# Kernel optimization log

Hardware: AMD Instinct MI355X
Metric: run time of the kernel (lower is better)

Reference implementation:

```python
import jax, jax.numpy as jnp
import numpy as np

CE_WEIGHT = 1.0
TRIPLET_WEIGHT = 0.1
MARGIN = 0.2


def setup_inputs() -> dict:
    key = jax.random.key(0)
    k1, k2, k3 = jax.random.split(key, 3)
    B, D, V = 4096, 512, 6000
    logits = jax.random.normal(k1, (B, V), dtype=jnp.float32)
    embeddings = jax.random.normal(k2, (B, D), dtype=jnp.float32)
    labels = jax.random.randint(k3, (B,), 0, 512, dtype=jnp.int64)
    return {"logits": logits, "embeddings": embeddings, "labels": labels}


def _pairwise_dist(emb):
    # Euclidean cdist via gram matrix; safe sqrt (zero grad where d2 == 0).
    sq = jnp.sum(emb * emb, axis=-1)  # [B]
    d2 = sq[:, None] + sq[None, :] - 2.0 * (emb @ emb.T)  # [B, B]
    d2 = jnp.maximum(d2, 0.0)
    safe = jnp.where(d2 > 0.0, d2, 1.0)
    return jnp.where(d2 > 0.0, jnp.sqrt(safe), 0.0)


def _losses(logits, embeddings, labels):
    B = logits.shape[0]
    # Cross entropy (mean reduction, matching nn.CrossEntropyLoss).
    logp = jax.nn.log_softmax(logits, axis=-1)
    ce_loss = -jnp.mean(jnp.take_along_axis(logp, labels[:, None], axis=1)[:, 0])

    # Batch-hard triplet loss, fully vectorized (one masked amax/amin per row).
    dist = _pairwise_dist(embeddings)  # [B, B]
    same = labels[:, None] == labels[None, :]  # [B, B]
    eye = jnp.eye(B, dtype=bool)
    pos_mask = same & ~eye
    neg_mask = ~same
    neg_inf = jnp.float32(-np.inf)
    pos_inf = jnp.float32(np.inf)
    hardest_pos = jnp.max(jnp.where(pos_mask, dist, neg_inf), axis=1)  # [B]
    hardest_neg = jnp.min(jnp.where(neg_mask, dist, pos_inf), axis=1)  # [B]
    valid = jnp.any(pos_mask, axis=1) & jnp.any(neg_mask, axis=1)  # [B]
    per_row = jax.nn.relu(hardest_pos - hardest_neg + MARGIN)
    per_row = jnp.where(valid, per_row, 0.0)
    n_valid = jnp.sum(valid.astype(jnp.float32))
    triplet_loss = jnp.where(n_valid > 0, jnp.sum(per_row) / jnp.maximum(n_valid, 1.0), 0.0)

    total_loss = CE_WEIGHT * ce_loss + TRIPLET_WEIGHT * triplet_loss
    return total_loss, ce_loss, triplet_loss


def reference(logits, embeddings, labels):
    return _losses(logits, embeddings, labels)
```

## Files before the change

kernel.cpp:

```cpp
#include <hip/hip_runtime.h>
#include <hip/hip_bf16.h>
#include <math.h>

#define BN   4096
#define DN   512
#define VN   6000
#define NCLS 512

typedef __attribute__((ext_vector_type(8)))  short short8;
typedef __attribute__((ext_vector_type(16))) float f32x16;

__device__ __forceinline__ unsigned short f2bf(float x) {
  unsigned int u = __float_as_uint(x);
  u = (u + 0x7FFFu + ((u >> 16) & 1u)) >> 16;
  return (unsigned short)u;
}

__device__ __forceinline__ void gld_lds16(const unsigned short* g, unsigned short* l) {
  __builtin_amdgcn_global_load_lds(
      (const __attribute__((address_space(1))) void*)g,
      (__attribute__((address_space(3))) void*)l, 16, 0, 0);
}

__launch_bounds__(256)
__global__ void prep_kernel(const float* __restrict__ emb, const int* __restrict__ labels,
                            unsigned short* __restrict__ embh, float* __restrict__ sqn,
                            int* __restrict__ cnt, int* __restrict__ posb,
                            int* __restrict__ negb) {
  const int row  = blockIdx.x * 4 + (threadIdx.x >> 6);
  const int lane = threadIdx.x & 63;
  const float4* rp = (const float4*)(emb + (size_t)row * DN);
  float4 a = rp[lane];
  float4 b = rp[lane + 64];
  float ss = a.x * a.x + a.y * a.y + a.z * a.z + a.w * a.w
           + b.x * b.x + b.y * b.y + b.z * b.z + b.w * b.w;
  ushort4 ha, hb;
  ha.x = f2bf(a.x); ha.y = f2bf(a.y); ha.z = f2bf(a.z); ha.w = f2bf(a.w);
  hb.x = f2bf(b.x); hb.y = f2bf(b.y); hb.z = f2bf(b.z); hb.w = f2bf(b.w);
  ushort4* wp = (ushort4*)(embh + (size_t)row * DN);
  wp[lane] = ha;
  wp[lane + 64] = hb;
#pragma unroll
  for (int off = 1; off < 64; off <<= 1) ss += __shfl_xor(ss, off);
  if (lane == 0) {
    sqn[row] = ss;
    posb[row] = 0;
    negb[row] = 0x7F800000;
    atomicAdd(cnt + labels[row], 1);
  }
}

__device__ __forceinline__ void triplet_job(int t, unsigned short* smem,
                                            const unsigned short* __restrict__ embh,
                                            const float* __restrict__ sqn,
                                            const int* __restrict__ labels,
                                            int* __restrict__ posb,
                                            int* __restrict__ negb, int lane) {
  const int m = lane & 31;
  const int half = lane >> 5;

  int J = (int)((sqrtf(8.f * (float)t + 1.f) - 1.f) * 0.5f);
  while ((J + 1) * (J + 2) / 2 <= t) ++J;
  while (J * (J + 1) / 2 > t) --J;
  const int I = t - J * (J + 1) / 2;
  const int i0 = I * 64, j0 = J * 64;
  const bool diag = (I == J);

  const int   li = labels[i0 + lane];
  const float qi = sqn[i0 + lane];
  const int   lj = labels[j0 + lane];
  const float qj = sqn[j0 + lane];

  const int lrow = lane >> 3;
  const int lchk = (lane & 7) ^ lrow;
  const unsigned short* gA = embh + (size_t)(i0 + lrow) * DN + lchk * 8;
  const unsigned short* gB = embh + (size_t)(j0 + lrow) * DN + lchk * 8;

  f32x16 acc[2][2] = {};
  f32x16 accT[2][2] = {};

#pragma unroll
  for (int s = 0; s < 8; ++s) {
    gld_lds16(gA + (size_t)s * 8 * DN, smem + s * 512);
    gld_lds16(gB + (size_t)s * 8 * DN, smem + 4096 + s * 512);
  }

  for (int ks = 0; ks < 8; ++ks) {
    const int cur = (ks & 1) * 8192;
    if (ks < 7) {
      const int nxt = 8192 - cur;
      const int kk = (ks + 1) * 64;
      asm volatile("s_waitcnt lgkmcnt(0)" ::: "memory");
#pragma unroll
      for (int s = 0; s < 8; ++s) {
        gld_lds16(gA + kk + (size_t)s * 8 * DN, smem + nxt + s * 512);
        gld_lds16(gB + kk + (size_t)s * 8 * DN, smem + nxt + 4096 + s * 512);
      }
      asm volatile("s_waitcnt vmcnt(16)" ::: "memory");
    } else {
      asm volatile("s_waitcnt vmcnt(0)" ::: "memory");
    }
    unsigned short* sA = smem + cur;
    unsigned short* sB = smem + cur + 4096;
#pragma unroll
    for (int q = 0; q < 4; ++q) {
      const int c = q * 2 + half;
      const int sw = ((c ^ (m & 7)) * 8);
      short8 a0 = *(const short8*)&sA[m * 64 + sw];
      short8 a1 = *(const short8*)&sA[(32 + m) * 64 + sw];
      short8 b0 = *(const short8*)&sB[m * 64 + sw];
      short8 b1 = *(const short8*)&sB[(32 + m) * 64 + sw];
      acc[0][0]  = __builtin_amdgcn_mfma_f32_32x32x16_bf16(a0, b0, acc[0][0], 0, 0, 0);
      acc[0][1]  = __builtin_amdgcn_mfma_f32_32x32x16_bf16(a0, b1, acc[0][1], 0, 0, 0);
      acc[1][0]  = __builtin_amdgcn_mfma_f32_32x32x16_bf16(a1, b0, acc[1][0], 0, 0, 0);
      acc[1][1]  = __builtin_amdgcn_mfma_f32_32x32x16_bf16(a1, b1, acc[1][1], 0, 0, 0);
      accT[0][0] = __builtin_amdgcn_mfma_f32_32x32x16_bf16(b0, a0, accT[0][0], 0, 0, 0);
      accT[0][1] = __builtin_amdgcn_mfma_f32_32x32x16_bf16(b0, a1, accT[0][1], 0, 0, 0);
      accT[1][0] = __builtin_amdgcn_mfma_f32_32x32x16_bf16(b1, a0, accT[1][0], 0, 0, 0);
      accT[1][1] = __builtin_amdgcn_mfma_f32_32x32x16_bf16(b1, a1, accT[1][1], 0, 0, 0);
    }
  }

  int*   sLab = (int*)smem;
  float* sQn  = (float*)(smem + 256);
  sLab[lane] = li;  sLab[64 + lane] = lj;
  sQn[lane]  = qi;  sQn[64 + lane]  = qj;
  asm volatile("s_waitcnt lgkmcnt(0)" ::: "memory");

  {
    const int gj0 = j0 + m, gj1 = j0 + 32 + m;
    const int cl0 = sLab[64 + m], cl1 = sLab[64 + 32 + m];
    const float cq0 = sQn[64 + m], cq1 = sQn[64 + 32 + m];
    float p0 = 0.f, p1 = 0.f, n0 = INFINITY, n1 = INFINITY;
#pragma unroll
    for (int rb = 0; rb < 2; ++rb) {
#pragma unroll
      for (int r = 0; r < 16; ++r) {
        const int ri = rb * 32 + (r & 3) + 8 * (r >> 2) + 4 * half;
        const int gi = i0 + ri;
        const int rl = sLab[ri];
        const float rq = sQn[ri];
        const float d0 = fmaf(-2.f, acc[rb][0][r], rq + cq0);
        const float d1 = fmaf(-2.f, acc[rb][1][r], rq + cq1);
        if (rl == cl0) { if (gi != gj0) p0 = fmaxf(p0, d0); } else n0 = fminf(n0, d0);
        if (rl == cl1) { if (gi != gj1) p1 = fmaxf(p1, d1); } else n1 = fminf(n1, d1);
      }
    }
    p0 = fmaxf(p0, __shfl_xor(p0, 32)); n0 = fminf(n0, __shfl_xor(n0, 32));
    p1 = fmaxf(p1, __shfl_xor(p1, 32)); n1 = fminf(n1, __shfl_xor(n1, 32));
    if (half == 0) {
      atomicMax(posb + gj0, __float_as_int(p0));
      atomicMin(negb + gj0, __float_as_int(n0));
      atomicMax(posb + gj1, __float_as_int(p1));
      atomicMin(negb + gj1, __float_as_int(n1));
    }
  }

  if (!diag) {
    const int gj0 = i0 + m, gj1 = i0 + 32 + m;
    const int cl0 = sLab[m], cl1 = sLab[32 + m];
    const float cq0 = sQn[m], cq1 = sQn[32 + m];
    float p0 = 0.f, p1 = 0.f, n0 = INFINITY, n1 = INFINITY;
#pragma unroll
    for (int rb = 0; rb < 2; ++rb) {
#pragma unroll
      for (int r = 0; r < 16; ++r) {
        const int rj = rb * 32 + (r & 3) + 8 * (r >> 2) + 4 * half;
        const int rl = sLab[64 + rj];
        const float rq = sQn[64 + rj];
        const float d0 = fmaf(-2.f, accT[rb][0][r], rq + cq0);
        const float d1 = fmaf(-2.f, accT[rb][1][r], rq + cq1);
        if (rl == cl0) p0 = fmaxf(p0, d0); else n0 = fminf(n0, d0);
        if (rl == cl1) p1 = fmaxf(p1, d1); else n1 = fminf(n1, d1);
      }
    }
    p0 = fmaxf(p0, __shfl_xor(p0, 32)); n0 = fminf(n0, __shfl_xor(n0, 32));
    p1 = fmaxf(p1, __shfl_xor(p1, 32)); n1 = fminf(n1, __shfl_xor(n1, 32));
    if (half == 0) {
      atomicMax(posb + gj0, __float_as_int(p0));
      atomicMin(negb + gj0, __float_as_int(n0));
      atomicMax(posb + gj1, __float_as_int(p1));
      atomicMin(negb + gj1, __float_as_int(n1));
    }
  }
}

__launch_bounds__(64, 2)
__global__ void fused_kernel(const float* __restrict__ logits,
                             const int* __restrict__ labels,
                             float* __restrict__ ce_part,
                             const unsigned short* __restrict__ embh,
                             const float* __restrict__ sqn,
                             int* __restrict__ posb, int* __restrict__ negb) {
  __shared__ unsigned short smem[16384];
  const int b = blockIdx.x;
  const int lane = threadIdx.x;

  int trip_job, ce_row;
  if (b < 32) {
    trip_job = 2048 + b; ce_row = -1;
  } else {
    const int g = (b - 32) / 3, r = (b - 32) % 3;
    if (r == 0) { trip_job = g; ce_row = -1; }
    else        { trip_job = -1; ce_row = g * 2 + (r - 1); }
  }

  if (trip_job >= 0) {
    triplet_job(trip_job, smem, embh, sqn, labels, posb, negb, lane);
    return;
  }

  const float* rp = logits + (size_t)ce_row * VN;
  const float xlab = rp[labels[ce_row]];
  const float4* q = (const float4*)rp;
  float4 v[24];
#pragma unroll
  for (int u = 0; u < 23; ++u) v[u] = q[lane + u * 64];
  if (lane < 28) v[23] = q[lane + 23 * 64];
  float s = 0.f;
#pragma unroll
  for (int u = 0; u < 23; ++u)
    s += __expf(v[u].x) + __expf(v[u].y) + __expf(v[u].z) + __expf(v[u].w);
  if (lane < 28)
    s += __expf(v[23].x) + __expf(v[23].y) + __expf(v[23].z) + __expf(v[23].w);
#pragma unroll
  for (int off = 1; off < 64; off <<= 1) s += __shfl_xor(s, off);
  if (lane == 0) ce_part[ce_row] = logf(s) - xlab;
}

__launch_bounds__(1024)
__global__ void finalize_kernel(const int* __restrict__ posb, const int* __restrict__ negb,
                                const int* __restrict__ labels, const int* __restrict__ cnt,
                                const float* __restrict__ ce_part, float* __restrict__ out) {
  const int tid = threadIdx.x;
  float cesum = 0.f, sum = 0.f, nv = 0.f;
#pragma unroll
  for (int u = 0; u < 4; ++u) {
    const int i = tid + u * 1024;
    cesum += ce_part[i];
    int c = cnt[labels[i]];
    float p = sqrtf(fmaxf(__int_as_float(posb[i]), 0.f));
    float n = sqrtf(fmaxf(__int_as_float(negb[i]), 0.f));
    float t = fmaxf(p - n + 0.2f, 0.f);
    if (c >= 2 && c < BN) { sum += t; nv += 1.f; }
  }
#pragma unroll
  for (int off = 1; off < 64; off <<= 1) {
    cesum += __shfl_xor(cesum, off);
    sum   += __shfl_xor(sum, off);
    nv    += __shfl_xor(nv, off);
  }
  __shared__ float s0[16], s1[16], s2[16];
  if ((tid & 63) == 0) { s0[tid >> 6] = cesum; s1[tid >> 6] = sum; s2[tid >> 6] = nv; }
  __syncthreads();
  if (tid == 0) {
    cesum = 0.f; sum = 0.f; nv = 0.f;
#pragma unroll
    for (int wv = 0; wv < 16; ++wv) { cesum += s0[wv]; sum += s1[wv]; nv += s2[wv]; }
    float trip = (nv > 0.f) ? sum / nv : 0.f;
    float ce = cesum * (1.f / BN);
    out[0] = ce + 0.1f * trip;
    out[1] = ce;
    out[2] = trip;
  }
}

extern "C" void kernel_launch(void* const* d_in, const int* in_sizes, int n_in,
                              void* d_out, int out_size, void* d_ws, size_t ws_size,
                              hipStream_t stream) {
  const float* logits = (const float*)d_in[0];
  const float* emb    = (const float*)d_in[1];
  const int*   labels = (const int*)d_in[2];
  float* out = (float*)d_out;

  char* ws = (char*)d_ws;
  unsigned short* embh = (unsigned short*)ws;
  float* sqn    = (float*)(ws + (size_t)BN * DN * 2);
  int*   posb   = (int*)((char*)sqn  + (size_t)BN * 4);
  int*   negb   = (int*)((char*)posb + (size_t)BN * 4);
  int*   cnt    = (int*)((char*)negb + (size_t)BN * 4);
  float* ce_part = (float*)((char*)cnt + (size_t)NCLS * 4);

  hipMemsetAsync(cnt, 0, (size_t)NCLS * 4, stream);
  hipLaunchKernelGGL(prep_kernel, dim3(BN / 4), dim3(256), 0, stream,
                     emb, labels, embh, sqn, cnt, posb, negb);
  hipLaunchKernelGGL(fused_kernel, dim3(32 + 2048 * 3), dim3(64), 0, stream,
                     logits, labels, ce_part, embh, sqn, posb, negb);
  hipLaunchKernelGGL(finalize_kernel, dim3(1), dim3(1024), 0, stream,
                     posb, negb, labels, cnt, ce_part, out);
}
```

Before: 179.2 us.

## Load MFMA operands directly from global into registers, drop LDS staging

The triplet Gram tile no longer stages bf16 embedding chunks through double-buffered LDS via global_load_lds. Each lane now loads its MFMA fragments straight from global memory into registers, with a 4-step software prefetch ring. LDS shrinks from 32KB to 1KB, which could allow more blocks to reside per CU. The cost is many short 16-byte strided global loads per lane instead of coalesced row loads, plus heavier register pressure from the fragment arrays.

```diff
diff --git a/kernel.cpp b/kernel.cpp
--- a/kernel.cpp
+++ b/kernel.cpp
@@ -14,12 +14,6 @@
   unsigned int u = __float_as_uint(x);
   u = (u + 0x7FFFu + ((u >> 16) & 1u)) >> 16;
   return (unsigned short)u;
-}
-
-__device__ __forceinline__ void gld_lds16(const unsigned short* g, unsigned short* l) {
-  __builtin_amdgcn_global_load_lds(
-      (const __attribute__((address_space(1))) void*)g,
-      (__attribute__((address_space(3))) void*)l, 16, 0, 0);
 }
 
 __launch_bounds__(256)
@@ -71,55 +65,40 @@
   const int   lj = labels[j0 + lane];
   const float qj = sqn[j0 + lane];
 
-  const int lrow = lane >> 3;
-  const int lchk = (lane & 7) ^ lrow;
-  const unsigned short* gA = embh + (size_t)(i0 + lrow) * DN + lchk * 8;
-  const unsigned short* gB = embh + (size_t)(j0 + lrow) * DN + lchk * 8;
+  const unsigned short* pa0 = embh + (size_t)(i0 + m)      * DN + half * 8;
+  const unsigned short* pa1 = embh + (size_t)(i0 + 32 + m) * DN + half * 8;
+  const unsigned short* pb0 = embh + (size_t)(j0 + m)      * DN + half * 8;
+  const unsigned short* pb1 = embh + (size_t)(j0 + 32 + m) * DN + half * 8;
 
   f32x16 acc[2][2] = {};
   f32x16 accT[2][2] = {};
 
-#pragma unroll
-  for (int s = 0; s < 8; ++s) {
-    gld_lds16(gA + (size_t)s * 8 * DN, smem + s * 512);
-    gld_lds16(gB + (size_t)s * 8 * DN, smem + 4096 + s * 512);
-  }
-
-  for (int ks = 0; ks < 8; ++ks) {
-    const int cur = (ks & 1) * 8192;
-    if (ks < 7) {
-      const int nxt = 8192 - cur;
-      const int kk = (ks + 1) * 64;
-      asm volatile("s_waitcnt lgkmcnt(0)" ::: "memory");
-#pragma unroll
-      for (int s = 0; s < 8; ++s) {
-        gld_lds16(gA + kk + (size_t)s * 8 * DN, smem + nxt + s * 512);
-        gld_lds16(gB + kk + (size_t)s * 8 * DN, smem + nxt + 4096 + s * 512);
-      }
-      asm volatile("s_waitcnt vmcnt(16)" ::: "memory");
-    } else {
-      asm volatile("s_waitcnt vmcnt(0)" ::: "memory");
-    }
-    unsigned short* sA = smem + cur;
-    unsigned short* sB = smem + cur + 4096;
-#pragma unroll
-    for (int q = 0; q < 4; ++q) {
-      const int c = q * 2 + half;
-      const int sw = ((c ^ (m & 7)) * 8);
-      short8 a0 = *(const short8*)&sA[m * 64 + sw];
-      short8 a1 = *(const short8*)&sA[(32 + m) * 64 + sw];
-      short8 b0 = *(const short8*)&sB[m * 64 + sw];
-      short8 b1 = *(const short8*)&sB[(32 + m) * 64 + sw];
-      acc[0][0]  = __builtin_amdgcn_mfma_f32_32x32x16_bf16(a0, b0, acc[0][0], 0, 0, 0);
-      acc[0][1]  = __builtin_amdgcn_mfma_f32_32x32x16_bf16(a0, b1, acc[0][1], 0, 0, 0);
-      acc[1][0]  = __builtin_amdgcn_mfma_f32_32x32x16_bf16(a1, b0, acc[1][0], 0, 0, 0);
-      acc[1][1]  = __builtin_amdgcn_mfma_f32_32x32x16_bf16(a1, b1, acc[1][1], 0, 0, 0);
-      accT[0][0] = __builtin_amdgcn_mfma_f32_32x32x16_bf16(b0, a0, accT[0][0], 0, 0, 0);
-      accT[0][1] = __builtin_amdgcn_mfma_f32_32x32x16_bf16(b0, a1, accT[0][1], 0, 0, 0);
-      accT[1][0] = __builtin_amdgcn_mfma_f32_32x32x16_bf16(b1, a0, accT[1][0], 0, 0, 0);
-      accT[1][1] = __builtin_amdgcn_mfma_f32_32x32x16_bf16(b1, a1, accT[1][1], 0, 0, 0);
-    }
-  }
+  short8 fa0[32], fa1[32], fb0[32], fb1[32];
+#define TJ_LOAD(s)                                                   \
+  do {                                                               \
+    fa0[s] = *(const short8*)(pa0 + (s) * 16);                       \
+    fa1[s] = *(const short8*)(pa1 + (s) * 16);                       \
+    fb0[s] = *(const short8*)(pb0 + (s) * 16);                       \
+    fb1[s] = *(const short8*)(pb1 + (s) * 16);                       \
+  } while (0)
+
+#pragma unroll
+  for (int s = 0; s < 4; ++s) TJ_LOAD(s);
+
+#pragma unroll
+  for (int s = 0; s < 32; ++s) {
+    if (s < 28) TJ_LOAD(s + 4);
+    const short8 a0 = fa0[s], a1 = fa1[s], b0 = fb0[s], b1 = fb1[s];
+    acc[0][0]  = __builtin_amdgcn_mfma_f32_32x32x16_bf16(a0, b0, acc[0][0], 0, 0, 0);
+    acc[0][1]  = __builtin_amdgcn_mfma_f32_32x32x16_bf16(a0, b1, acc[0][1], 0, 0, 0);
+    acc[1][0]  = __builtin_amdgcn_mfma_f32_32x32x16_bf16(a1, b0, acc[1][0], 0, 0, 0);
+    acc[1][1]  = __builtin_amdgcn_mfma_f32_32x32x16_bf16(a1, b1, acc[1][1], 0, 0, 0);
+    accT[0][0] = __builtin_amdgcn_mfma_f32_32x32x16_bf16(b0, a0, accT[0][0], 0, 0, 0);
+    accT[0][1] = __builtin_amdgcn_mfma_f32_32x32x16_bf16(b0, a1, accT[0][1], 0, 0, 0);
+    accT[1][0] = __builtin_amdgcn_mfma_f32_32x32x16_bf16(b1, a0, accT[1][0], 0, 0, 0);
+    accT[1][1] = __builtin_amdgcn_mfma_f32_32x32x16_bf16(b1, a1, accT[1][1], 0, 0, 0);
+  }
+#undef TJ_LOAD
 
   int*   sLab = (int*)smem;
   float* sQn  = (float*)(smem + 256);
@@ -192,7 +171,7 @@
                              const unsigned short* __restrict__ embh,
                              const float* __restrict__ sqn,
                              int* __restrict__ posb, int* __restrict__ negb) {
-  __shared__ unsigned short smem[16384];
+  __shared__ unsigned short smem[512];
   const int b = blockIdx.x;
   const int lane = threadIdx.x;
 
```

New measurement: 199.5 us. +11.3%, slower.
